# Performance work log

Measured on AMD Instinct MI355X. Metric: run time of the kernel, lower is better.

## Reference

```python
import jax, jax.numpy as jnp
import numpy as np

D, HEADS, HD, L, P, DFF = 256, 8, 32, 4, 4, 2048
B, NQ = 4, 900
SHAPES = [(128, 128), (64, 64), (32, 32), (16, 16)]
S = sum(h * w for h, w in SHAPES)


def setup_inputs():
    ks = iter(jax.random.split(jax.random.key(0), 20))
    rn = lambda *s: jax.random.normal(next(ks), s, jnp.float32) * 0.02
    cxcy = jax.random.uniform(next(ks), (B, NQ, 1, 2), minval=0.1, maxval=0.9)
    wh = jax.random.uniform(next(ks), (B, NQ, 1, 2), minval=0.05, maxval=0.3)
    ref = jnp.broadcast_to(jnp.concatenate([cxcy, wh], -1), (B, NQ, L, 4))
    starts = np.cumsum([0] + [h * w for h, w in SHAPES[:-1]])
    return dict(
        query=jax.random.normal(next(ks), (B, NQ, D), jnp.float32),
        query_pos=jax.random.normal(next(ks), (B, NQ, D), jnp.float32),
        reference_points=ref,
        input_flatten=jax.random.normal(next(ks), (B, S, D), jnp.float32),
        input_spatial_shapes=jnp.array(SHAPES, jnp.int32),
        input_level_start_index=jnp.array(starts, jnp.int32),
        sa_in_w=rn(3, D, D), sa_in_b=jnp.zeros((3, D)),
        sa_out_w=rn(D, D), sa_out_b=jnp.zeros((D,)),
        norm1_g=jnp.ones((D,)), norm1_b=jnp.zeros((D,)),
        value_w=rn(D, D), value_b=jnp.zeros((D,)),
        off_w=rn(D, HEADS * L * P * 2),
        off_b=jax.random.uniform(next(ks), (HEADS * L * P * 2,), minval=-1.0, maxval=1.0),
        aw_w=rn(D, HEADS * L * P), aw_b=jnp.zeros((HEADS * L * P,)),
        ca_out_w=rn(D, D), ca_out_b=jnp.zeros((D,)),
        norm2_g=jnp.ones((D,)), norm2_b=jnp.zeros((D,)),
        lin1_w=rn(D, DFF), lin1_b=jnp.zeros((DFF,)),
        lin2_w=rn(DFF, D), lin2_b=jnp.zeros((D,)),
        norm3_g=jnp.ones((D,)), norm3_b=jnp.zeros((D,)),
    )


def _ln(x, g, b, eps=1e-5):
    m = x.mean(-1, keepdims=True)
    v = ((x - m) ** 2).mean(-1, keepdims=True)
    return (x - m) * jax.lax.rsqrt(v + eps) * g + b


def _msdeform(q, input_flatten, ref, shapes, starts, value_w, value_b,
              off_w, off_b, aw_w, aw_b, out_w, out_b):
    Bq, Nq, _ = q.shape
    # value: (B, heads, S, head_dim)
    v = (input_flatten @ value_w + value_b).reshape(Bq, -1, HEADS, HD).transpose(0, 2, 1, 3)
    off = (q @ off_w + off_b).reshape(Bq, Nq, HEADS, L, P, 2).transpose(0, 2, 1, 3, 4, 5)
    aw = jax.nn.softmax((q @ aw_w + aw_b).reshape(Bq, Nq, HEADS, L * P), axis=-1)
    aw = aw.reshape(Bq, Nq, HEADS, L, P).transpose(0, 2, 1, 3, 4)  # (B,H,Nq,L,P)
    refc = ref[:, None, :, :, None, :]  # (B,1,Nq,L,1,4)
    # box refs: center + offset/P * wh * 0.5  (Deformable-DETR convention)
    loc = refc[..., :2] + off / P * refc[..., 2:] * 0.5  # (B,H,Nq,L,P,2)
    out = jnp.zeros((Bq, HEADS, Nq, HD), q.dtype)
    for l, (H, W) in enumerate(shapes):
        vl = jax.lax.dynamic_slice_in_dim(v, starts[l], H * W, axis=2)  # (B,H,HW,hd)
        x = loc[:, :, :, l, :, 0] * W - 0.5  # align_corners=False pixel coords
        y = loc[:, :, :, l, :, 1] * H - 0.5
        x0, y0 = jnp.floor(x), jnp.floor(y)
        dx, dy = x - x0, y - y0

        def g(xi, yi):
            valid = (xi >= 0) & (xi < W) & (yi >= 0) & (yi < H)  # zero padding
            idx = (jnp.clip(yi, 0, H - 1) * W + jnp.clip(xi, 0, W - 1)).astype(jnp.int32)
            gat = jnp.take_along_axis(vl, idx.reshape(Bq, HEADS, Nq * P, 1), axis=2)
            return gat.reshape(Bq, HEADS, Nq, P, HD) * valid[..., None]

        samp = (((1 - dx) * (1 - dy))[..., None] * g(x0, y0)
                + (dx * (1 - dy))[..., None] * g(x0 + 1, y0)
                + ((1 - dx) * dy)[..., None] * g(x0, y0 + 1)
                + (dx * dy)[..., None] * g(x0 + 1, y0 + 1))
        out = out + jnp.sum(aw[:, :, :, l, :, None] * samp, axis=3)
    return out.transpose(0, 2, 1, 3).reshape(Bq, Nq, D) @ out_w + out_b


def _layer(query, query_pos, reference_points, input_flatten, shapes, starts, p):
    Bq, Nq, _ = query.shape
    qk = query + query_pos
    heads = lambda x: x.reshape(Bq, Nq, HEADS, HD).transpose(0, 2, 1, 3)
    qh = heads(qk @ p['sa_in_w'][0] + p['sa_in_b'][0])
    kh = heads(qk @ p['sa_in_w'][1] + p['sa_in_b'][1])
    vh = heads(query @ p['sa_in_w'][2] + p['sa_in_b'][2])
    attn = jax.nn.softmax(jnp.einsum('bhqd,bhkd->bhqk', qh, kh) * (HD ** -0.5), axis=-1)
    sa = jnp.einsum('bhqk,bhkd->bhqd', attn, vh).transpose(0, 2, 1, 3).reshape(Bq, Nq, D)
    sa = sa @ p['sa_out_w'] + p['sa_out_b']
    x = _ln(query + sa, p['norm1_g'], p['norm1_b'])
    ca = _msdeform(x + query_pos, input_flatten, reference_points, shapes, starts,
                   p['value_w'], p['value_b'], p['off_w'], p['off_b'],
                   p['aw_w'], p['aw_b'], p['ca_out_w'], p['ca_out_b'])
    x = _ln(x + ca, p['norm2_g'], p['norm2_b'])
    ffn = jax.nn.relu(x @ p['lin1_w'] + p['lin1_b']) @ p['lin2_w'] + p['lin2_b']
    return _ln(x + ffn, p['norm3_g'], p['norm3_b'])


PNAMES = ['sa_in_w', 'sa_in_b', 'sa_out_w', 'sa_out_b', 'norm1_g', 'norm1_b',
          'value_w', 'value_b', 'off_w', 'off_b', 'aw_w', 'aw_b',
          'ca_out_w', 'ca_out_b', 'norm2_g', 'norm2_b',
          'lin1_w', 'lin1_b', 'lin2_w', 'lin2_b', 'norm3_g', 'norm3_b']


def reference(query, query_pos, reference_points, input_flatten,
              input_spatial_shapes, input_level_start_index,
              sa_in_w, sa_in_b, sa_out_w, sa_out_b, norm1_g, norm1_b,
              value_w, value_b, off_w, off_b, aw_w, aw_b,
              ca_out_w, ca_out_b, norm2_g, norm2_b,
              lin1_w, lin1_b, lin2_w, lin2_b, norm3_g, norm3_b):
    # spatial shapes / start indices are static structural metadata
    shapes = [(int(h), int(w)) for h, w in np.asarray(input_spatial_shapes)]
    starts = [int(s) for s in np.asarray(input_level_start_index)]
    p = dict(zip(PNAMES, (sa_in_w, sa_in_b, sa_out_w, sa_out_b, norm1_g, norm1_b,
                          value_w, value_b, off_w, off_b, aw_w, aw_b,
                          ca_out_w, ca_out_b, norm2_g, norm2_b,
                          lin1_w, lin1_b, lin2_w, lin2_b, norm3_g, norm3_b)))
    return _layer(query, query_pos, reference_points, input_flatten, shapes, starts, p)
```

## Files before the change

kernel.cpp:

```cpp
#include <hip/hip_runtime.h>
#include <hip/hip_bf16.h>

#define DD   256
#define NH   8
#define HDIM 32
#define LV   4
#define NP   4
#define DFF  2048
#define BB   4
#define NQQ  900
#define SS   21760

typedef __bf16 bf16x8 __attribute__((ext_vector_type(8)));
typedef __bf16 bf16x2 __attribute__((ext_vector_type(2)));
typedef float  f32x4  __attribute__((ext_vector_type(4)));

__device__ inline void stval(float* p, float v) { *p = v; }
__device__ inline void stval(__bf16* p, float v) { *p = (__bf16)v; }

__device__ __forceinline__ void gload16(const void* g, void* l) {
    __builtin_amdgcn_global_load_lds(
        (const __attribute__((address_space(1))) void*)g,
        (__attribute__((address_space(3))) void*)l, 16, 0, 0);
}

struct TPtrs {
    const float* s[10];
    __bf16* d[10];
};

__global__ void transp_all(TPtrs P) {
    const int Ks[10] = {256, 256, 256, 256, 256, 256, 256, 256, 256, 2048};
    const int Ns[10] = {256, 256, 256, 256, 256, 256, 128, 256, 2048, 256};
    const int tiles[10] = {64, 64, 64, 64, 64, 64, 32, 64, 512, 512};
    int t = blockIdx.x;
    int j = 0, base = 0;
    while (t >= base + tiles[j]) { base += tiles[j]; j++; }
    int lt = t - base;
    int K = Ks[j], N = Ns[j];
    int tn = N >> 5;
    int nb = (lt % tn) * 32, kb = (lt / tn) * 32;
    const float* W = P.s[j];
    __bf16* Wt = P.d[j];
    __shared__ float tbuf[32][33];
    for (int i = threadIdx.y; i < 32; i += 8)
        tbuf[i][threadIdx.x] = W[(size_t)(kb + i) * N + nb + threadIdx.x];
    __syncthreads();
    for (int i = threadIdx.y; i < 32; i += 8)
        Wt[(size_t)(nb + i) * K + kb + threadIdx.x] = (__bf16)tbuf[threadIdx.x][i];
}

#define BM 64
#define BN 64
#define BKK 64

template <typename AT, typename OT, int RELU, int NSUB, bool LNF>
__device__ __forceinline__ void gemm_body(
    int bx, int by, char* ldsraw,
    const AT* __restrict__ A, const float* __restrict__ A2,
    const __bf16* __restrict__ Wt,
    const float* __restrict__ bias, const float* __restrict__ bias2, int nsplit,
    const float* __restrict__ res, const float* __restrict__ lng,
    const float* __restrict__ lnb,
    OT* __restrict__ C, int M, int N, int K) {
    int tid = threadIdx.x;
    int lane = tid & 63;
    int wave = tid >> 6;
    int wr = wave >> 1, wc = wave & 1;
    int m0 = by * BM;
    int n0 = bx * (BN * NSUB);

    __bf16* As = (__bf16*)ldsraw;
    __bf16* Bs = (__bf16*)(ldsraw + BM * BKK * 2);
    float* rsum  = (float*)(ldsraw + BM * BKK * 2 + NSUB * BN * BKK * 2);
    float* rsum2 = rsum + 128;

    f32x4 acc[NSUB][2][2] = {};

    int srow = tid >> 2;
    int sq = tid & 3;
    int u0 = sq << 1;
    int p0 = (u0 ^ (srow & 7)) * 8;
    int p1 = ((u0 + 1) ^ (srow & 7)) * 8;
    int fr = lane & 15, gq = lane >> 4;

    for (int k0 = 0; k0 < K; k0 += BKK) {
        {
            int gm = m0 + srow;
            bf16x8 v0 = {}, v1 = {};
            if (gm < M) {
                if constexpr (sizeof(AT) == 4) {
                    const float* ap = (const float*)A + (size_t)gm * K + k0 + sq * 16;
                    f32x4 f0 = *(const f32x4*)(ap + 0);
                    f32x4 f1 = *(const f32x4*)(ap + 4);
                    f32x4 f2 = *(const f32x4*)(ap + 8);
                    f32x4 f3 = *(const f32x4*)(ap + 12);
                    if (A2) {
                        const float* ap2 = A2 + (size_t)gm * K + k0 + sq * 16;
                        f0 += *(const f32x4*)(ap2 + 0);
                        f1 += *(const f32x4*)(ap2 + 4);
                        f2 += *(const f32x4*)(ap2 + 8);
                        f3 += *(const f32x4*)(ap2 + 12);
                    }
#pragma unroll
                    for (int e = 0; e < 4; e++) {
                        v0[e] = (__bf16)f0[e]; v0[e + 4] = (__bf16)f1[e];
                        v1[e] = (__bf16)f2[e]; v1[e + 4] = (__bf16)f3[e];
                    }
                } else {
                    const __bf16* ap = (const __bf16*)A + (size_t)gm * K + k0 + sq * 16;
                    v0 = *(const bf16x8*)(ap);
                    v1 = *(const bf16x8*)(ap + 8);
                }
            }
            *(bf16x8*)(&As[srow * 64 + p0]) = v0;
            *(bf16x8*)(&As[srow * 64 + p1]) = v1;
        }
#pragma unroll
        for (int ns = 0; ns < NSUB; ns++) {
            int gn = n0 + ns * BN + srow;
            const __bf16* bp = Wt + (size_t)gn * K + k0 + sq * 16;
            bf16x8 w0 = *(const bf16x8*)(bp);
            bf16x8 w1 = *(const bf16x8*)(bp + 8);
            *(bf16x8*)(&Bs[ns * BN * BKK + srow * 64 + p0]) = w0;
            *(bf16x8*)(&Bs[ns * BN * BKK + srow * 64 + p1]) = w1;
        }
        __syncthreads();
#pragma unroll
        for (int ks = 0; ks < 2; ks++) {
            bf16x8 a[2];
#pragma unroll
            for (int i = 0; i < 2; i++) {
                int ma = wr * 32 + i * 16 + fr;
                a[i] = *(const bf16x8*)(&As[ma * 64 + ((ks * 4 + gq) ^ (ma & 7)) * 8]);
            }
#pragma unroll
            for (int ns = 0; ns < NSUB; ns++) {
                bf16x8 b[2];
#pragma unroll
                for (int j = 0; j < 2; j++) {
                    int nb = wc * 32 + j * 16 + fr;
                    b[j] = *(const bf16x8*)(&Bs[ns * BN * BKK + nb * 64 + ((ks * 4 + gq) ^ (nb & 7)) * 8]);
                }
#pragma unroll
                for (int i = 0; i < 2; i++)
#pragma unroll
                    for (int j = 0; j < 2; j++)
                        acc[ns][i][j] = __builtin_amdgcn_mfma_f32_16x16x32_bf16(a[i], b[j], acc[ns][i][j], 0, 0, 0);
            }
        }
        __syncthreads();
    }
    int orow = gq * 4;
    if constexpr (!LNF) {
#pragma unroll
        for (int ns = 0; ns < NSUB; ns++)
#pragma unroll
            for (int i = 0; i < 2; i++)
#pragma unroll
                for (int j = 0; j < 2; j++) {
                    int gn = n0 + ns * BN + wc * 32 + j * 16 + fr;
                    float bv = (gn < nsplit) ? bias[gn] : bias2[gn - nsplit];
#pragma unroll
                    for (int r = 0; r < 4; r++) {
                        int gm = m0 + wr * 32 + i * 16 + orow + r;
                        if (gm < M) {
                            float v = acc[ns][i][j][r] + bv;
                            if (RELU) v = fmaxf(v, 0.f);
                            stval(C + (size_t)gm * N + gn, v);
                        }
                    }
                }
    } else {
        float part[2][4] = {};
#pragma unroll
        for (int ns = 0; ns < NSUB; ns++)
#pragma unroll
            for (int i = 0; i < 2; i++)
#pragma unroll
                for (int j = 0; j < 2; j++) {
                    int gn = ns * BN + wc * 32 + j * 16 + fr;
                    float bv = bias[gn];
#pragma unroll
                    for (int r = 0; r < 4; r++) {
                        int gm = m0 + wr * 32 + i * 16 + orow + r;
                        float rv = (gm < M) ? res[(size_t)gm * 256 + gn] : 0.f;
                        float x = acc[ns][i][j][r] + bv + rv;
                        acc[ns][i][j][r] = x;
                        part[i][r] += x;
                    }
                }
#pragma unroll
        for (int i = 0; i < 2; i++)
#pragma unroll
            for (int r = 0; r < 4; r++) {
                float v = part[i][r];
                v += __shfl_xor(v, 1);
                v += __shfl_xor(v, 2);
                v += __shfl_xor(v, 4);
                v += __shfl_xor(v, 8);
                part[i][r] = v;
            }
        if (fr == 0) {
#pragma unroll
            for (int i = 0; i < 2; i++)
#pragma unroll
                for (int r = 0; r < 4; r++)
                    rsum[(wr * 32 + i * 16 + orow + r) * 2 + wc] = part[i][r];
        }
        __syncthreads();
        float mean[2][4];
#pragma unroll
        for (int i = 0; i < 2; i++)
#pragma unroll
            for (int r = 0; r < 4; r++) {
                int rl = wr * 32 + i * 16 + orow + r;
                mean[i][r] = (rsum[rl * 2] + rsum[rl * 2 + 1]) * (1.f / 256.f);
            }
        float p2[2][4] = {};
#pragma unroll
        for (int ns = 0; ns < NSUB; ns++)
#pragma unroll
            for (int i = 0; i < 2; i++)
#pragma unroll
                for (int j = 0; j < 2; j++)
#pragma unroll
                    for (int r = 0; r < 4; r++) {
                        float d = acc[ns][i][j][r] - mean[i][r];
                        p2[i][r] += d * d;
                    }
#pragma unroll
        for (int i = 0; i < 2; i++)
#pragma unroll
            for (int r = 0; r < 4; r++) {
                float v = p2[i][r];
                v += __shfl_xor(v, 1);
                v += __shfl_xor(v, 2);
                v += __shfl_xor(v, 4);
                v += __shfl_xor(v, 8);
                p2[i][r] = v;
            }
        if (fr == 0) {
#pragma unroll
            for (int i = 0; i < 2; i++)
#pragma unroll
                for (int r = 0; r < 4; r++)
                    rsum2[(wr * 32 + i * 16 + orow + r) * 2 + wc] = p2[i][r];
        }
        __syncthreads();
        float rstd[2][4];
#pragma unroll
        for (int i = 0; i < 2; i++)
#pragma unroll
            for (int r = 0; r < 4; r++) {
                int rl = wr * 32 + i * 16 + orow + r;
                float var = (rsum2[rl * 2] + rsum2[rl * 2 + 1]) * (1.f / 256.f);
                rstd[i][r] = rsqrtf(var + 1e-5f);
            }
#pragma unroll
        for (int ns = 0; ns < NSUB; ns++)
#pragma unroll
            for (int i = 0; i < 2; i++)
#pragma unroll
                for (int j = 0; j < 2; j++) {
                    int gn = ns * BN + wc * 32 + j * 16 + fr;
                    float gv = lng[gn], bev = lnb[gn];
#pragma unroll
                    for (int r = 0; r < 4; r++) {
                        int gm = m0 + wr * 32 + i * 16 + orow + r;
                        if (gm < M) {
                            float y = (acc[ns][i][j][r] - mean[i][r]) * rstd[i][r] * gv + bev;
                            stval(C + (size_t)gm * 256 + gn, y);
                        }
                    }
                }
    }
}

template <typename AT, typename OT, int RELU, int NSUB, bool LNF>
__global__ __launch_bounds__(256) void mfma_gemm(
    const AT* __restrict__ A, const float* __restrict__ A2,
    const __bf16* __restrict__ Wt,
    const float* __restrict__ bias, const float* __restrict__ bias2, int nsplit,
    const float* __restrict__ res, const float* __restrict__ lng,
    const float* __restrict__ lnb,
    OT* __restrict__ C, int M, int N, int K) {
    __shared__ __attribute__((aligned(16))) char lds[BM * BKK * 2 + NSUB * BN * BKK * 2 + (LNF ? 1024 : 0)];
    gemm_body<AT, OT, RELU, NSUB, LNF>(blockIdx.x, blockIdx.y, lds, A, A2, Wt,
                                       bias, bias2, nsplit, res, lng, lnb, C, M, N, K);
}

__device__ __forceinline__ void value_body(
    int bx, char* ldsraw,
    const float* __restrict__ A, const __bf16* __restrict__ Wt,
    const float* __restrict__ bias, __bf16* __restrict__ C) {
    int tid = threadIdx.x;
    int lane = tid & 63;
    int wave = tid >> 6;
    int fr = lane & 15, gq = lane >> 4;
    int m0 = bx * 64;

    __bf16* As = (__bf16*)ldsraw;
    __bf16* Bq = (__bf16*)(ldsraw + 16384);

    f32x4 acc[4][4] = {};

    int srow = tid >> 2;
    int sq = tid & 3;
    int u0 = sq << 1;
    int p0 = (u0 ^ (srow & 7)) * 8;
    int p1 = ((u0 + 1) ^ (srow & 7)) * 8;

    int c_row = lane >> 3;
    int c_u = lane & 7;
    int gu = c_u ^ c_row;
    const __bf16* bsrc0 = Wt + (size_t)(wave * 64 + c_row) * 256 + gu * 8;
    const float* aptr = A + (size_t)(m0 + srow) * 256 + sq * 16;

    f32x4 fA0, fA1, fA2, fA3;
    f32x4 fB0, fB1, fB2, fB3;

#define LOADA(s0_, s1_, s2_, s3_, off)                          \
    { const float* _p = aptr + (off);                           \
      s0_ = *(const f32x4*)(_p + 0);  s1_ = *(const f32x4*)(_p + 4); \
      s2_ = *(const f32x4*)(_p + 8);  s3_ = *(const f32x4*)(_p + 12); }

#define WRITEA(buf, s0_, s1_, s2_, s3_)                         \
    { bf16x8 _v0, _v1;                                          \
      _Pragma("unroll")                                         \
      for (int e = 0; e < 4; e++) {                             \
          _v0[e] = (__bf16)s0_[e]; _v0[e + 4] = (__bf16)s1_[e]; \
          _v1[e] = (__bf16)s2_[e]; _v1[e + 4] = (__bf16)s3_[e]; \
      }                                                         \
      *(bf16x8*)(&As[(buf) * 4096 + srow * 64 + p0]) = _v0;     \
      *(bf16x8*)(&As[(buf) * 4096 + srow * 64 + p1]) = _v1; }

#define ISSUEB(step, buf)                                       \
    { const __bf16* _b = bsrc0 + (step) * 64;                   \
      _Pragma("unroll")                                         \
      for (int c = 0; c < 8; c++)                               \
          gload16(_b + (size_t)c * 8 * 256, &Bq[((buf) * 4 + wave) * 4096 + c * 512]); }

#define MFMAS(buf)                                              \
    _Pragma("unroll")                                           \
    for (int ks = 0; ks < 2; ks++) {                            \
        bf16x8 a[4], b[4];                                      \
        _Pragma("unroll")                                       \
        for (int i = 0; i < 4; i++) {                           \
            int ma = i * 16 + fr;                               \
            a[i] = *(const bf16x8*)(&As[(buf) * 4096 + ma * 64 + ((ks * 4 + gq) ^ (ma & 7)) * 8]); \
            b[i] = *(const bf16x8*)(&Bq[((buf) * 4 + wave) * 4096 + ma * 64 + ((ks * 4 + gq) ^ (ma & 7)) * 8]); \
        }                                                       \
        _Pragma("unroll")                                       \
        for (int i = 0; i < 4; i++)                             \
            _Pragma("unroll")                                   \
            for (int j = 0; j < 4; j++)                         \
                acc[i][j] = __builtin_amdgcn_mfma_f32_16x16x32_bf16(a[i], b[j], acc[i][j], 0, 0, 0); \
    }

    LOADA(fA0, fA1, fA2, fA3, 0);
    __builtin_amdgcn_sched_barrier(0);
    ISSUEB(0, 0);
    LOADA(fB0, fB1, fB2, fB3, 64);
    asm volatile("s_waitcnt vmcnt(12)" ::: "memory");
    __builtin_amdgcn_sched_barrier(0);
    WRITEA(0, fA0, fA1, fA2, fA3);
    asm volatile("s_waitcnt lgkmcnt(0)" ::: "memory");
    __builtin_amdgcn_s_barrier();

    ISSUEB(1, 1);
    LOADA(fA0, fA1, fA2, fA3, 128);
    asm volatile("s_waitcnt vmcnt(16)" ::: "memory");
    __builtin_amdgcn_sched_barrier(0);
    MFMAS(0);
    asm volatile("s_waitcnt vmcnt(12)" ::: "memory");
    __builtin_amdgcn_sched_barrier(0);
    WRITEA(1, fB0, fB1, fB2, fB3);
    asm volatile("s_waitcnt lgkmcnt(0)" ::: "memory");
    __builtin_amdgcn_s_barrier();

    ISSUEB(2, 0);
    LOADA(fB0, fB1, fB2, fB3, 192);
    asm volatile("s_waitcnt vmcnt(16)" ::: "memory");
    __builtin_amdgcn_sched_barrier(0);
    MFMAS(1);
    asm volatile("s_waitcnt vmcnt(12)" ::: "memory");
    __builtin_amdgcn_sched_barrier(0);
    WRITEA(0, fA0, fA1, fA2, fA3);
    asm volatile("s_waitcnt lgkmcnt(0)" ::: "memory");
    __builtin_amdgcn_s_barrier();

    ISSUEB(3, 1);
    asm volatile("s_waitcnt vmcnt(12)" ::: "memory");
    __builtin_amdgcn_sched_barrier(0);
    MFMAS(0);
    asm volatile("s_waitcnt vmcnt(8)" ::: "memory");
    __builtin_amdgcn_sched_barrier(0);
    WRITEA(1, fB0, fB1, fB2, fB3);
    asm volatile("s_waitcnt lgkmcnt(0)" ::: "memory");
    __builtin_amdgcn_s_barrier();

    asm volatile("s_waitcnt vmcnt(0)" ::: "memory");
    __builtin_amdgcn_sched_barrier(0);
    MFMAS(1);

#undef LOADA
#undef WRITEA
#undef ISSUEB
#undef MFMAS

#pragma unroll
    for (int i = 0; i < 4; i++)
#pragma unroll
        for (int j = 0; j < 4; j++) {
            int gn = wave * 64 + j * 16 + fr;
            float bv = bias[gn];
#pragma unroll
            for (int r = 0; r < 4; r++) {
                int gm = m0 + i * 16 + gq * 4 + r;
                C[(size_t)gm * 256 + gn] = (__bf16)(acc[i][j][r] + bv);
            }
        }
}

#define NVALB 1360
#define NQKB  228
#define NVB   228

__global__ __launch_bounds__(256) void fused_head(
    const float* __restrict__ input_flat, const __bf16* __restrict__ wt_val,
    const float* __restrict__ value_b, __bf16* __restrict__ vbig,
    const float* __restrict__ query, const float* __restrict__ query_pos,
    const __bf16* __restrict__ wt_q, const float* __restrict__ sa_in_b,
    __bf16* __restrict__ qkbuf, const __bf16* __restrict__ wt_v,
    __bf16* __restrict__ Vp, int M) {
    __shared__ __attribute__((aligned(16))) char lds[81920];
    int bx = blockIdx.x;
    if (bx < NVALB) {
        value_body(bx, lds, input_flat, wt_val, value_b, vbig);
    } else if (bx < NVALB + NQKB) {
        int b2 = bx - NVALB;
        gemm_body<float, __bf16, 0, 2, false>(b2 & 3, b2 >> 2, lds,
            query, query_pos, wt_q, sa_in_b, sa_in_b, 1 << 30,
            nullptr, nullptr, nullptr, qkbuf, M, 512, 256);
    } else {
        int b2 = bx - NVALB - NQKB;
        gemm_body<float, __bf16, 0, 1, false>(b2 & 3, b2 >> 2, lds,
            query, nullptr, wt_v, sa_in_b + 512, sa_in_b, 1 << 30,
            nullptr, nullptr, nullptr, Vp, M, 256, 256);
    }
}

__global__ void fillmark(float* o, int n, float v) {
    int i = blockIdx.x * blockDim.x + threadIdx.x;
    if (i < n) o[i] = v;
}

__global__ void ln_res(const float* a, const float* b,
                       const float* g, const float* be, float* o) {
    int row = blockIdx.x;
    int t = threadIdx.x;
    float x = a[(size_t)row * DD + t] + b[(size_t)row * DD + t];
    __shared__ float red[DD];
    red[t] = x;
    __syncthreads();
    for (int s = 128; s > 0; s >>= 1) {
        if (t < s) red[t] += red[t + s];
        __syncthreads();
    }
    float m = red[0] * (1.f / DD);
    __syncthreads();
    float d0 = x - m;
    red[t] = d0 * d0;
    __syncthreads();
    for (int s = 128; s > 0; s >>= 1) {
        if (t < s) red[t] += red[t + s];
        __syncthreads();
    }
    float v = red[0] * (1.f / DD);
    o[(size_t)row * DD + t] = d0 * rsqrtf(v + 1e-5f) * g[t] + be[t];
}

#define QT 64
#define KT 64
#define NT ((NQQ + KT - 1) / KT)
#define QKLD 512

__global__ __launch_bounds__(256) void sa_attn_mfma(
    const __bf16* __restrict__ QK, const __bf16* __restrict__ V,
    float* __restrict__ O) {
    int blk = blockIdx.x;
    int tq = blk % NT;
    int bh = blk / NT;
    int h = bh % NH;
    int b = bh / NH;
    int tid = threadIdx.x;
    int lane = tid & 63;
    int wave = tid >> 6;
    int fr = lane & 15, gq = lane >> 4;
    int q0 = tq * QT;

    __shared__ __attribute__((aligned(16))) __bf16 Ks[KT][56];
    __shared__ __attribute__((aligned(16))) __bf16 Vt[HDIM][72];
    __shared__ __attribute__((aligned(16))) __bf16 Ps[4][16][72];

    int qrow = q0 + wave * 16 + fr;
    bf16x8 aq = {};
    if (qrow < NQQ)
        aq = *(const bf16x8*)(QK + ((size_t)(b * NQQ + qrow)) * QKLD + h * HDIM + gq * 8);

    f32x4 o0 = {}, o1 = {};
    float m_r[4] = {-1e30f, -1e30f, -1e30f, -1e30f};
    float l_r[4] = {0.f, 0.f, 0.f, 0.f};
    const float scale = 0.17677669529663687f;

    for (int kt = 0; kt < NT; kt++) {
        int kv0 = kt * KT;
        {
            int r = tid >> 2;
            int c8 = (tid & 3) * 8;
            int kvr = kv0 + r;
            bf16x8 kv_ = {}, vv_ = {};
            if (kvr < NQQ) {
                kv_ = *(const bf16x8*)(QK + ((size_t)(b * NQQ + kvr)) * QKLD + 256 + h * HDIM + c8);
                vv_ = *(const bf16x8*)(V + ((size_t)(b * NQQ + kvr)) * DD + h * HDIM + c8);
            }
            *(bf16x8*)(&Ks[r][c8]) = kv_;
#pragma unroll
            for (int j = 0; j < 8; j++) Vt[c8 + j][r] = vv_[j];
        }
        __syncthreads();

        f32x4 s[4];
#pragma unroll
        for (int f = 0; f < 4; f++) {
            bf16x8 bk = *(const bf16x8*)(&Ks[f * 16 + fr][gq * 8]);
            f32x4 z = {};
            s[f] = __builtin_amdgcn_mfma_f32_16x16x32_bf16(aq, bk, z, 0, 0, 0);
        }
#pragma unroll
        for (int f = 0; f < 4; f++) {
            bool valid = (kv0 + f * 16 + fr) < NQQ;
#pragma unroll
            for (int r = 0; r < 4; r++)
                s[f][r] = valid ? s[f][r] * scale : -1e30f;
        }
        float sc_[4];
#pragma unroll
        for (int r = 0; r < 4; r++) {
            float v = fmaxf(fmaxf(s[0][r], s[1][r]), fmaxf(s[2][r], s[3][r]));
            v = fmaxf(v, __shfl_xor(v, 1));
            v = fmaxf(v, __shfl_xor(v, 2));
            v = fmaxf(v, __shfl_xor(v, 4));
            v = fmaxf(v, __shfl_xor(v, 8));
            float mn = fmaxf(m_r[r], v);
            sc_[r] = expf(m_r[r] - mn);
            m_r[r] = mn;
        }
        float rs[4] = {0.f, 0.f, 0.f, 0.f};
#pragma unroll
        for (int f = 0; f < 4; f++)
#pragma unroll
            for (int r = 0; r < 4; r++) {
                float e = expf(s[f][r] - m_r[r]);
                s[f][r] = e;
                rs[r] += e;
            }
#pragma unroll
        for (int r = 0; r < 4; r++) {
            float v = rs[r];
            v += __shfl_xor(v, 1);
            v += __shfl_xor(v, 2);
            v += __shfl_xor(v, 4);
            v += __shfl_xor(v, 8);
            l_r[r] = l_r[r] * sc_[r] + v;
            o0[r] *= sc_[r];
            o1[r] *= sc_[r];
        }
#pragma unroll
        for (int f = 0; f < 4; f++)
#pragma unroll
            for (int r = 0; r < 4; r++)
                Ps[wave][gq * 4 + r][f * 16 + fr] = (__bf16)s[f][r];
#pragma unroll
        for (int c = 0; c < 2; c++) {
            bf16x8 ap = *(const bf16x8*)(&Ps[wave][fr][c * 32 + gq * 8]);
            bf16x8 bv0 = *(const bf16x8*)(&Vt[fr][c * 32 + gq * 8]);
            bf16x8 bv1 = *(const bf16x8*)(&Vt[16 + fr][c * 32 + gq * 8]);
            o0 = __builtin_amdgcn_mfma_f32_16x16x32_bf16(ap, bv0, o0, 0, 0, 0);
            o1 = __builtin_amdgcn_mfma_f32_16x16x32_bf16(ap, bv1, o1, 0, 0, 0);
        }
        __syncthreads();
    }
#pragma unroll
    for (int r = 0; r < 4; r++) {
        int qr = q0 + wave * 16 + gq * 4 + r;
        if (qr < NQQ) {
            float inv = 1.f / l_r[r];
            O[((size_t)(b * NQQ + qr)) * DD + h * HDIM + fr] = o0[r] * inv;
            O[((size_t)(b * NQQ + qr)) * DD + h * HDIM + 16 + fr] = o1[r] * inv;
        }
    }
}

#define OAW 384

__global__ __launch_bounds__(256) void msdeform3(
    const __bf16* __restrict__ val, const __bf16* __restrict__ oa,
    const float* __restrict__ ref, float* __restrict__ out) {
    int tid = threadIdx.x;
    int row = blockIdx.x;
    int b_ = row / NQQ;

    __shared__ float sx[128], sy[128], sw[128];

    if (tid < 128) {
        int h = tid >> 4;
        int lp = tid & 15;
        int l = lp >> 2;
        float logit = (float)oa[(size_t)row * OAW + 256 + h * 16 + lp];
        float ox = (float)oa[(size_t)row * OAW + h * 32 + lp * 2];
        float oy = (float)oa[(size_t)row * OAW + h * 32 + lp * 2 + 1];
        const float* rp = ref + ((size_t)row * LV + l) * 4;
        float cx = rp[0], cy = rp[1], rw = rp[2], rh = rp[3];
        float mv = logit;
        mv = fmaxf(mv, __shfl_xor(mv, 1));
        mv = fmaxf(mv, __shfl_xor(mv, 2));
        mv = fmaxf(mv, __shfl_xor(mv, 4));
        mv = fmaxf(mv, __shfl_xor(mv, 8));
        float e = expf(logit - mv);
        float sum = e;
        sum += __shfl_xor(sum, 1);
        sum += __shfl_xor(sum, 2);
        sum += __shfl_xor(sum, 4);
        sum += __shfl_xor(sum, 8);
        int Wl = 128 >> l;
        float lx = cx + ox * (1.0f / NP) * rw * 0.5f;
        float ly = cy + oy * (1.0f / NP) * rh * 0.5f;
        sx[tid] = lx * Wl - 0.5f;
        sy[tid] = ly * Wl - 0.5f;
        sw[tid] = e / sum;
    }
    __syncthreads();

    int cpar = tid & 7;
    int dgrp = (tid >> 3) & 3;
    int h = tid >> 5;
    const int stt[4] = {0, 16384, 20480, 21504};
    const __bf16* vb = val + (size_t)b_ * SS * DD + h * HDIM + dgrp * 8;
    float facc[8] = {};
#pragma unroll
    for (int k = 0; k < 8; k++) {
        int combo = cpar * 8 + k;
        int lp = combo >> 2;
        int tap = combo & 3;
        int l = lp >> 2;
        int Wl = 128 >> l;
        int cidx = h * 16 + lp;
        float x = sx[cidx], y = sy[cidx], w = sw[cidx];
        float x0f = floorf(x), y0f = floorf(y);
        float dx = x - x0f, dy = y - y0f;
        int xi = (int)x0f + (tap & 1);
        int yi = (int)y0f + (tap >> 1);
        float wt = ((tap & 1) ? dx : 1.f - dx) * ((tap >> 1) ? dy : 1.f - dy) * w;
        if ((xi >= 0) & (xi < Wl) & (yi >= 0) & (yi < Wl)) {
            bf16x8 t = *(const bf16x8*)(vb + (size_t)(stt[l] + yi * Wl + xi) * DD);
#pragma unroll
            for (int e = 0; e < 8; e++) facc[e] += wt * (float)t[e];
        }
    }
#pragma unroll
    for (int e = 0; e < 8; e++) {
        facc[e] += __shfl_xor(facc[e], 1);
        facc[e] += __shfl_xor(facc[e], 2);
        facc[e] += __shfl_xor(facc[e], 4);
    }
    float v = facc[0];
#pragma unroll
    for (int e = 1; e < 8; e++) if (cpar == e) v = facc[e];
    out[(size_t)row * DD + tid] = v;
}

extern "C" void kernel_launch(void* const* d_in, const int* in_sizes, int n_in,
                              void* d_out, int out_size, void* d_ws, size_t ws_size,
                              hipStream_t stream) {
    const float* query      = (const float*)d_in[0];
    const float* query_pos  = (const float*)d_in[1];
    const float* refpts     = (const float*)d_in[2];
    const float* input_flat = (const float*)d_in[3];
    const float* sa_in_w    = (const float*)d_in[6];
    const float* sa_in_b    = (const float*)d_in[7];
    const float* sa_out_w   = (const float*)d_in[8];
    const float* sa_out_b   = (const float*)d_in[9];
    const float* norm1_g    = (const float*)d_in[10];
    const float* norm1_b    = (const float*)d_in[11];
    const float* value_w    = (const float*)d_in[12];
    const float* value_b    = (const float*)d_in[13];
    const float* off_w      = (const float*)d_in[14];
    const float* off_b      = (const float*)d_in[15];
    const float* aw_w       = (const float*)d_in[16];
    const float* aw_b       = (const float*)d_in[17];
    const float* ca_out_w   = (const float*)d_in[18];
    const float* ca_out_b   = (const float*)d_in[19];
    const float* norm2_g    = (const float*)d_in[20];
    const float* norm2_b    = (const float*)d_in[21];
    const float* lin1_w     = (const float*)d_in[22];
    const float* lin1_b     = (const float*)d_in[23];
    const float* lin2_w     = (const float*)d_in[24];
    const float* lin2_b     = (const float*)d_in[25];
    const float* norm3_g    = (const float*)d_in[26];
    const float* norm3_b    = (const float*)d_in[27];
    float* out = (float*)d_out;

    const int M = BB * NQQ;
    const int NE = M * DD;
    const size_t slotBytes = (size_t)NE * 4;
    const size_t wElems = 6 * 65536 + 32768 + 65536 + 2 * 524288;
    const size_t wBytes = wElems * 2;
    const size_t bigBytes = (size_t)BB * SS * DD * 2;
    const size_t needBytes = 3 * slotBytes + wBytes + bigBytes;
    if (ws_size < needBytes) {
        float mark = 1000.0f + (float)(ws_size >> 20);
        fillmark<<<(out_size + 255) / 256, 256, 0, stream>>>(out, out_size, mark);
        return;
    }

    char* wsb = (char*)d_ws;
    float* s0 = (float*)(wsb);
    float* s1 = (float*)(wsb + slotBytes);
    float* s2 = (float*)(wsb + 2 * slotBytes);
    __bf16* wb = (__bf16*)(wsb + 3 * slotBytes);
    __bf16* vbig = (__bf16*)(wsb + 3 * slotBytes + wBytes);

    __bf16* wt_q   = wb;
    __bf16* wt_k   = wb + 65536;
    __bf16* wt_v   = wb + 131072;
    __bf16* wt_sa  = wb + 196608;
    __bf16* wt_val = wb + 262144;
    __bf16* wt_off = wb + 327680;
    __bf16* wt_aw  = wb + 393216;
    __bf16* wt_ca  = wb + 425984;
    __bf16* wt_l1  = wb + 491520;
    __bf16* wt_l2  = wb + 1015808;

    TPtrs tp;
    tp.s[0] = sa_in_w;          tp.d[0] = wt_q;
    tp.s[1] = sa_in_w + 65536;  tp.d[1] = wt_k;
    tp.s[2] = sa_in_w + 131072; tp.d[2] = wt_v;
    tp.s[3] = sa_out_w;         tp.d[3] = wt_sa;
    tp.s[4] = value_w;          tp.d[4] = wt_val;
    tp.s[5] = off_w;            tp.d[5] = wt_off;
    tp.s[6] = aw_w;             tp.d[6] = wt_aw;
    tp.s[7] = ca_out_w;         tp.d[7] = wt_ca;
    tp.s[8] = lin1_w;           tp.d[8] = wt_l1;
    tp.s[9] = lin2_w;           tp.d[9] = wt_l2;
    transp_all<<<1504, dim3(32, 8), 0, stream>>>(tp);

    __bf16* qkbuf = (__bf16*)s1;
    __bf16* Vp = (__bf16*)s2;
    __bf16* oabuf = (__bf16*)s1;

    const int mt = (M + BM - 1) / BM;
    const int BIG = 1 << 30;

    fused_head<<<NVALB + NQKB + NVB, 256, 0, stream>>>(
        input_flat, wt_val, value_b, vbig,
        query, query_pos, wt_q, sa_in_b, qkbuf, wt_v, Vp, M);
    sa_attn_mfma<<<BB * NH * NT, 256, 0, stream>>>(qkbuf, Vp, s0);
    mfma_gemm<float, float, 0, 4, true><<<dim3(1, mt), 256, 0, stream>>>(
        s0, nullptr, wt_sa, sa_out_b, sa_out_b, BIG,
        query, norm1_g, norm1_b, s2, M, DD, DD);
    mfma_gemm<float, __bf16, 0, 1, false><<<dim3(6, mt), 256, 0, stream>>>(
        s2, query_pos, wt_off, off_b, aw_b, 256,
        nullptr, nullptr, nullptr, oabuf, M, OAW, DD);
    msdeform3<<<M, 256, 0, stream>>>(vbig, oabuf, refpts, s0);
    mfma_gemm<float, float, 0, 4, true><<<dim3(1, mt), 256, 0, stream>>>(
        s0, nullptr, wt_ca, ca_out_b, ca_out_b, BIG,
        s2, norm2_g, norm2_b, s1, M, DD, DD);
    mfma_gemm<float, __bf16, 1, 2, false><<<dim3(16, mt), 256, 0, stream>>>(
        s1, nullptr, wt_l1, lin1_b, lin1_b, BIG,
        nullptr, nullptr, nullptr, vbig, M, DFF, DD);
    mfma_gemm<__bf16, float, 0, 1, false><<<dim3(4, mt), 256, 0, stream>>>(
        vbig, nullptr, wt_l2, lin2_b, lin2_b, BIG,
        nullptr, nullptr, nullptr, s0, M, DD, DFF);
    ln_res<<<M, DD, 0, stream>>>(s1, s0, norm3_g, norm3_b, out);
}
```

Measured before the change: 203.7 us.

## Split-K the FFN second GEMM into two halves and reduce in LayerNorm

```diff
diff --git a/kernel.cpp b/kernel.cpp
--- a/kernel.cpp
+++ b/kernel.cpp
@@ -62,7 +62,7 @@
     const float* __restrict__ bias, const float* __restrict__ bias2, int nsplit,
     const float* __restrict__ res, const float* __restrict__ lng,
     const float* __restrict__ lnb,
-    OT* __restrict__ C, int M, int N, int K) {
+    OT* __restrict__ C, int M, int N, int K, int lda, int ldb, int kbeg) {
     int tid = threadIdx.x;
     int lane = tid & 63;
     int wave = tid >> 6;
@@ -90,13 +90,13 @@
             bf16x8 v0 = {}, v1 = {};
             if (gm < M) {
                 if constexpr (sizeof(AT) == 4) {
-                    const float* ap = (const float*)A + (size_t)gm * K + k0 + sq * 16;
+                    const float* ap = (const float*)A + (size_t)gm * lda + kbeg + k0 + sq * 16;
                     f32x4 f0 = *(const f32x4*)(ap + 0);
                     f32x4 f1 = *(const f32x4*)(ap + 4);
                     f32x4 f2 = *(const f32x4*)(ap + 8);
                     f32x4 f3 = *(const f32x4*)(ap + 12);
                     if (A2) {
-                        const float* ap2 = A2 + (size_t)gm * K + k0 + sq * 16;
+                        const float* ap2 = A2 + (size_t)gm * lda + kbeg + k0 + sq * 16;
                         f0 += *(const f32x4*)(ap2 + 0);
                         f1 += *(const f32x4*)(ap2 + 4);
                         f2 += *(const f32x4*)(ap2 + 8);
@@ -108,7 +108,7 @@
                         v1[e] = (__bf16)f2[e]; v1[e + 4] = (__bf16)f3[e];
                     }
                 } else {
-                    const __bf16* ap = (const __bf16*)A + (size_t)gm * K + k0 + sq * 16;
+                    const __bf16* ap = (const __bf16*)A + (size_t)gm * lda + kbeg + k0 + sq * 16;
                     v0 = *(const bf16x8*)(ap);
                     v1 = *(const bf16x8*)(ap + 8);
                 }
@@ -119,7 +119,7 @@
 #pragma unroll
         for (int ns = 0; ns < NSUB; ns++) {
             int gn = n0 + ns * BN + srow;
-            const __bf16* bp = Wt + (size_t)gn * K + k0 + sq * 16;
+            const __bf16* bp = Wt + (size_t)gn * ldb + kbeg + k0 + sq * 16;
             bf16x8 w0 = *(const bf16x8*)(bp);
             bf16x8 w1 = *(const bf16x8*)(bp + 8);
             *(bf16x8*)(&Bs[ns * BN * BKK + srow * 64 + p0]) = w0;
@@ -160,7 +160,7 @@
 #pragma unroll
                 for (int j = 0; j < 2; j++) {
                     int gn = n0 + ns * BN + wc * 32 + j * 16 + fr;
-                    float bv = (gn < nsplit) ? bias[gn] : bias2[gn - nsplit];
+                    float bv = bias ? ((gn < nsplit) ? bias[gn] : bias2[gn - nsplit]) : 0.f;
 #pragma unroll
                     for (int r = 0; r < 4; r++) {
                         int gm = m0 + wr * 32 + i * 16 + orow + r;
@@ -287,7 +287,20 @@
     OT* __restrict__ C, int M, int N, int K) {
     __shared__ __attribute__((aligned(16))) char lds[BM * BKK * 2 + NSUB * BN * BKK * 2 + (LNF ? 1024 : 0)];
     gemm_body<AT, OT, RELU, NSUB, LNF>(blockIdx.x, blockIdx.y, lds, A, A2, Wt,
-                                       bias, bias2, nsplit, res, lng, lnb, C, M, N, K);
+                                       bias, bias2, nsplit, res, lng, lnb, C, M, N, K, K, K, 0);
+}
+
+__global__ __launch_bounds__(256) void ffn2_split(
+    const __bf16* __restrict__ vbig, const __bf16* __restrict__ wt_l2,
+    float* __restrict__ p1, float* __restrict__ p2, int M) {
+    __shared__ __attribute__((aligned(16))) char lds[BM * BKK * 2 + BN * BKK * 2];
+    int bx = blockIdx.x;
+    int col = bx & 3;
+    int half = bx >> 2;
+    float* outp = half ? p2 : p1;
+    gemm_body<__bf16, float, 0, 1, false>(col, blockIdx.y, lds,
+        vbig, nullptr, wt_l2, nullptr, nullptr, 1 << 30,
+        nullptr, nullptr, nullptr, outp, M, 256, 1024, 2048, 2048, half * 1024);
 }
 
 __device__ __forceinline__ void value_body(
@@ -442,12 +455,12 @@
         int b2 = bx - NVALB;
         gemm_body<float, __bf16, 0, 2, false>(b2 & 3, b2 >> 2, lds,
             query, query_pos, wt_q, sa_in_b, sa_in_b, 1 << 30,
-            nullptr, nullptr, nullptr, qkbuf, M, 512, 256);
+            nullptr, nullptr, nullptr, qkbuf, M, 512, 256, 256, 256, 0);
     } else {
         int b2 = bx - NVALB - NQKB;
         gemm_body<float, __bf16, 0, 1, false>(b2 & 3, b2 >> 2, lds,
             query, nullptr, wt_v, sa_in_b + 512, sa_in_b, 1 << 30,
-            nullptr, nullptr, nullptr, Vp, M, 256, 256);
+            nullptr, nullptr, nullptr, Vp, M, 256, 256, 256, 256, 0);
     }
 }
 
@@ -456,11 +469,13 @@
     if (i < n) o[i] = v;
 }
 
-__global__ void ln_res(const float* a, const float* b,
-                       const float* g, const float* be, float* o) {
+__global__ void ln_res3(const float* a, const float* b1, const float* b2,
+                        const float* cb, const float* g, const float* be,
+                        float* o) {
     int row = blockIdx.x;
     int t = threadIdx.x;
-    float x = a[(size_t)row * DD + t] + b[(size_t)row * DD + t];
+    float x = a[(size_t)row * DD + t] + b1[(size_t)row * DD + t] +
+              b2[(size_t)row * DD + t] + cb[t];
     __shared__ float red[DD];
     red[t] = x;
     __syncthreads();
@@ -718,7 +733,7 @@
     const size_t wElems = 6 * 65536 + 32768 + 65536 + 2 * 524288;
     const size_t wBytes = wElems * 2;
     const size_t bigBytes = (size_t)BB * SS * DD * 2;
-    const size_t needBytes = 3 * slotBytes + wBytes + bigBytes;
+    const size_t needBytes = 4 * slotBytes + wBytes + bigBytes;
     if (ws_size < needBytes) {
         float mark = 1000.0f + (float)(ws_size >> 20);
         fillmark<<<(out_size + 255) / 256, 256, 0, stream>>>(out, out_size, mark);
@@ -729,8 +744,9 @@
     float* s0 = (float*)(wsb);
     float* s1 = (float*)(wsb + slotBytes);
     float* s2 = (float*)(wsb + 2 * slotBytes);
-    __bf16* wb = (__bf16*)(wsb + 3 * slotBytes);
-    __bf16* vbig = (__bf16*)(wsb + 3 * slotBytes + wBytes);
+    float* s3 = (float*)(wsb + 3 * slotBytes);
+    __bf16* wb = (__bf16*)(wsb + 4 * slotBytes);
+    __bf16* vbig = (__bf16*)(wsb + 4 * slotBytes + wBytes);
 
     __bf16* wt_q   = wb;
     __bf16* wt_k   = wb + 65536;
@@ -769,19 +785,17 @@
     sa_attn_mfma<<<BB * NH * NT, 256, 0, stream>>>(qkbuf, Vp, s0);
     mfma_gemm<float, float, 0, 4, true><<<dim3(1, mt), 256, 0, stream>>>(
         s0, nullptr, wt_sa, sa_out_b, sa_out_b, BIG,
-        query, norm1_g, norm1_b, s2, M, DD, DD);
+        query, norm1_g, norm1_b, s3, M, DD, DD);
     mfma_gemm<float, __bf16, 0, 1, false><<<dim3(6, mt), 256, 0, stream>>>(
-        s2, query_pos, wt_off, off_b, aw_b, 256,
+        s3, query_pos, wt_off, off_b, aw_b, 256,
         nullptr, nullptr, nullptr, oabuf, M, OAW, DD);
     msdeform3<<<M, 256, 0, stream>>>(vbig, oabuf, refpts, s0);
     mfma_gemm<float, float, 0, 4, true><<<dim3(1, mt), 256, 0, stream>>>(
         s0, nullptr, wt_ca, ca_out_b, ca_out_b, BIG,
-        s2, norm2_g, norm2_b, s1, M, DD, DD);
+        s3, norm2_g, norm2_b, s1, M, DD, DD);
     mfma_gemm<float, __bf16, 1, 2, false><<<dim3(16, mt), 256, 0, stream>>>(
         s1, nullptr, wt_l1, lin1_b, lin1_b, BIG,
         nullptr, nullptr, nullptr, vbig, M, DFF, DD);
-    mfma_gemm<__bf16, float, 0, 1, false><<<dim3(4, mt), 256, 0, stream>>>(
-        vbig, nullptr, wt_l2, lin2_b, lin2_b, BIG,
-        nullptr, nullptr, nullptr, s0, M, DD, DFF);
-    ln_res<<<M, DD, 0, stream>>>(s1, s0, norm3_g, norm3_b, out);
-}
+    ffn2_split<<<dim3(8, mt), 256, 0, stream>>>(vbig, wt_l2, s0, s2, M);
+    ln_res3<<<M, DD, 0, stream>>>(s1, s0, s2, lin2_b, norm3_g, norm3_b, out);
+}
```

Measured after the change: 193.2 us. -5.2%, faster.
